# Kernel tuning notes

Measured on AMD Instinct MI355X. Metric: run time of the kernel, lower is better.

## Reference

```python
import jax, jax.numpy as jnp
import numpy as np

D_MODEL = 512
N_HEADS = 8
D_K = D_MODEL // N_HEADS
WINDOW = 64
SCALE = 1.0 / np.sqrt(D_K)


def setup_inputs() -> dict:
    key = jax.random.key(0)
    ks = jax.random.split(key, 9)
    B, S = 1, 2048
    s = 1.0 / np.sqrt(D_MODEL)
    inp = {
        "x": jax.random.normal(ks[0], (B, S, D_MODEL), dtype=jnp.float32),
        "Wq": jax.random.normal(ks[1], (D_MODEL, D_MODEL), dtype=jnp.float32) * s,
        "bq": jnp.zeros((D_MODEL,), dtype=jnp.float32),
        "Wk": jax.random.normal(ks[2], (D_MODEL, D_MODEL), dtype=jnp.float32) * s,
        "bk": jnp.zeros((D_MODEL,), dtype=jnp.float32),
        "Wv": jax.random.normal(ks[3], (D_MODEL, D_MODEL), dtype=jnp.float32) * s,
        "bv": jnp.zeros((D_MODEL,), dtype=jnp.float32),
        "Wo": jax.random.normal(ks[4], (D_MODEL, D_MODEL), dtype=jnp.float32) * s,
        "bo": jnp.zeros((D_MODEL,), dtype=jnp.float32),
    }
    return inp


def reference(x, Wq, bq, Wk, bk, Wv, bv, Wo, bo):
    B, S, _ = x.shape
    # projections (torch Linear: x @ W.T + b); split heads -> [B,S,H,dk]
    q = (x @ Wq.T + bq).reshape(B, S, N_HEADS, D_K)
    k = (x @ Wk.T + bk).reshape(B, S, N_HEADS, D_K)
    v = (x @ Wv.T + bv).reshape(B, S, N_HEADS, D_K)

    # banded window indices: position i attends to [i-W, i+W]
    L = 2 * WINDOW + 1
    offsets = jnp.arange(L) - WINDOW                    # [L]
    pos = jnp.arange(S)[:, None] + offsets[None, :]     # [S, L]
    valid = (pos >= 0) & (pos < S)                      # [S, L]
    posc = jnp.clip(pos, 0, S - 1)

    k_w = k[:, posc]                                    # [B, S, L, H, dk]
    v_w = v[:, posc]                                    # [B, S, L, H, dk]

    scores = jnp.einsum("bshd,bslhd->bhsl", q, k_w) * SCALE
    scores = jnp.where(valid[None, None, :, :], scores, -jnp.inf)
    attn = jax.nn.softmax(scores, axis=-1)              # [B, H, S, L]
    out = jnp.einsum("bhsl,bslhd->bshd", attn, v_w)     # [B, S, H, dk]
    out = out.reshape(B, S, D_MODEL)
    return out @ Wo.T + bo
```

## Files before the change

### kernel.cpp

```cpp
#include <hip/hip_runtime.h>
#include <hip/hip_bf16.h>
#include <math.h>

#define S_LEN  2048
#define DMODEL 512
#define NHEADS 8
#define DK     64
#define WIN    64

static constexpr float SCALE = 0.125f;

typedef short bf16x8 __attribute__((ext_vector_type(8)));
typedef float f32x4  __attribute__((ext_vector_type(4)));

__device__ __forceinline__ short bfh(float v)
{
    __hip_bfloat16 b = __float2bfloat16(v);
    return *reinterpret_cast<short*>(&b);
}
__device__ __forceinline__ float bf2f(short s)
{
    __hip_bfloat16 b = *reinterpret_cast<__hip_bfloat16*>(&s);
    return __bfloat162float(b);
}
__device__ __forceinline__ void split1(float v, short& h, short& l)
{
    h = bfh(v);
    l = bfh(v - bf2f(h));
}

__device__ __forceinline__ void dma16(const void* g, void* l)
{
    __builtin_amdgcn_global_load_lds(
        (const __attribute__((address_space(1))) unsigned int*)g,
        (__attribute__((address_space(3))) unsigned int*)l, 16, 0, 0);
}

__global__ __launch_bounds__(256)
void cast_ws(const float* __restrict__ x,  const float* __restrict__ wq,
             const float* __restrict__ wk, const float* __restrict__ wv,
             const float* __restrict__ wo,
             short* __restrict__ xh, short* __restrict__ xl,
             short* __restrict__ wqb, short* __restrict__ wkb,
             short* __restrict__ wvb, short* __restrict__ wob)
{
    const int z = blockIdx.z;
    if (z == 0) {
        for (int i = blockIdx.x * 256 + threadIdx.x; i < 262144; i += gridDim.x * 256) {
            const float4 v = ((const float4*)x)[i];
            short4 h, l;
            split1(v.x, h.x, l.x);
            split1(v.y, h.y, l.y);
            split1(v.z, h.z, l.z);
            split1(v.w, h.w, l.w);
            ((short4*)xh)[i] = h;
            ((short4*)xl)[i] = l;
        }
    } else {
        const float* s; short* d;
        switch (z) {
            case 1:  s = wq; d = wqb; break;
            case 2:  s = wk; d = wkb; break;
            case 3:  s = wv; d = wvb; break;
            default: s = wo; d = wob; break;
        }
        for (int i = blockIdx.x * 256 + threadIdx.x; i < 65536; i += gridDim.x * 256) {
            const float4 v = ((const float4*)s)[i];
            short4 o;
            o.x = bfh(v.x); o.y = bfh(v.y); o.z = bfh(v.z); o.w = bfh(v.w);
            ((short4*)d)[i] = o;
        }
    }
}

__global__ __launch_bounds__(128)
void gemm_qkv3(const short* __restrict__ xh, const short* __restrict__ xl,
               const short* __restrict__ wqb, const short* __restrict__ wkb,
               const short* __restrict__ wvb,
               const float* __restrict__ bq, const float* __restrict__ bk,
               const float* __restrict__ bv,
               short* __restrict__ qh, short* __restrict__ ql,
               short* __restrict__ kb, short* __restrict__ vbt)
{
    __shared__ __align__(16) short sB[64 * 256];

    const int z = blockIdx.z;
    const short* Bg   = (z == 0) ? wqb : (z == 1) ? wkb : wvb;
    const float* bias = (z == 0) ? bq  : (z == 1) ? bk  : bv;
    const int row0 = blockIdx.y * 64;
    const int col0 = blockIdx.x * 64;
    const int tid  = threadIdx.x;
    const int lane = tid & 63;
    const int wv   = tid >> 6;
    const int col  = lane & 15;
    const int quad = lane >> 4;

    f32x4 acc[2][4];
#pragma unroll
    for (int mi = 0; mi < 2; ++mi)
#pragma unroll
        for (int nj = 0; nj < 4; ++nj)
            acc[mi][nj] = (f32x4)0.0f;

    for (int ph = 0; ph < 2; ++ph) {
        __syncthreads();
        for (int i = wv; i < 32; i += 2) {
            const int q = i * 64 + lane;
            const int r = q >> 5;
            const int b = q & 31;
            const int j = b ^ (r & 7);
            dma16(Bg + (size_t)(col0 + r) * 512 + ph * 256 + j * 8, sB + i * 512);
        }
        __syncthreads();

#pragma unroll
        for (int kc = 0; kc < 8; ++kc) {
            const int k = ph * 256 + kc * 32;
            bf16x8 ah[2], al[2];
#pragma unroll
            for (int mi = 0; mi < 2; ++mi) {
                const int m = row0 + wv * 32 + mi * 16 + col;
                ah[mi] = *(const bf16x8*)(xh + (size_t)m * 512 + k + quad * 8);
                al[mi] = *(const bf16x8*)(xl + (size_t)m * 512 + k + quad * 8);
            }
#pragma unroll
            for (int nj = 0; nj < 4; ++nj) {
                const int n = nj * 16 + col;
                const int j = (kc * 4 + quad) ^ (n & 7);
                const bf16x8 bf = *(const bf16x8*)&sB[n * 256 + j * 8];
#pragma unroll
                for (int mi = 0; mi < 2; ++mi) {
                    acc[mi][nj] = __builtin_amdgcn_mfma_f32_16x16x32_bf16(ah[mi], bf, acc[mi][nj], 0, 0, 0);
                    acc[mi][nj] = __builtin_amdgcn_mfma_f32_16x16x32_bf16(al[mi], bf, acc[mi][nj], 0, 0, 0);
                }
            }
        }
    }

#pragma unroll
    for (int nj = 0; nj < 4; ++nj) {
        const int cc = col0 + nj * 16 + col;
        const float bias_v = bias[cc];
#pragma unroll
        for (int mi = 0; mi < 2; ++mi) {
#pragma unroll
            for (int e = 0; e < 4; ++e) {
                const int row = row0 + wv * 32 + mi * 16 + quad * 4 + e;
                const float val = acc[mi][nj][e] + bias_v;
                if (z == 0) {
                    short hh, ll;
                    split1(val, hh, ll);
                    qh[(size_t)row * 512 + cc] = hh;
                    ql[(size_t)row * 512 + cc] = ll;
                } else if (z == 1) {
                    kb[(size_t)row * 512 + cc] = bfh(val);
                } else {
                    vbt[(size_t)cc * 2048 + row] = bfh(val);
                }
            }
        }
    }
}

__global__ __launch_bounds__(128)
void gemm_out3(const short* __restrict__ ah_g, const short* __restrict__ al_g,
               const short* __restrict__ wob, const float* __restrict__ bo,
               float* __restrict__ out)
{
    __shared__ __align__(16) short sB[64 * 256];

    const int row0 = blockIdx.y * 32;
    const int col0 = blockIdx.x * 64;
    const int tid  = threadIdx.x;
    const int lane = tid & 63;
    const int wv   = tid >> 6;
    const int col  = lane & 15;
    const int quad = lane >> 4;

    f32x4 acc[4];
#pragma unroll
    for (int nj = 0; nj < 4; ++nj)
        acc[nj] = (f32x4)0.0f;

    for (int ph = 0; ph < 2; ++ph) {
        __syncthreads();
        for (int i = wv; i < 32; i += 2) {
            const int q = i * 64 + lane;
            const int r = q >> 5;
            const int b = q & 31;
            const int j = b ^ (r & 7);
            dma16(wob + (size_t)(col0 + r) * 512 + ph * 256 + j * 8, sB + i * 512);
        }
        __syncthreads();

#pragma unroll
        for (int kc = 0; kc < 8; ++kc) {
            const int k = ph * 256 + kc * 32;
            const int m = row0 + wv * 16 + col;
            const bf16x8 ah = *(const bf16x8*)(ah_g + (size_t)m * 512 + k + quad * 8);
            const bf16x8 al = *(const bf16x8*)(al_g + (size_t)m * 512 + k + quad * 8);
#pragma unroll
            for (int nj = 0; nj < 4; ++nj) {
                const int n = nj * 16 + col;
                const int j = (kc * 4 + quad) ^ (n & 7);
                const bf16x8 bf = *(const bf16x8*)&sB[n * 256 + j * 8];
                acc[nj] = __builtin_amdgcn_mfma_f32_16x16x32_bf16(ah, bf, acc[nj], 0, 0, 0);
                acc[nj] = __builtin_amdgcn_mfma_f32_16x16x32_bf16(al, bf, acc[nj], 0, 0, 0);
            }
        }
    }

#pragma unroll
    for (int nj = 0; nj < 4; ++nj) {
        const int cc = col0 + nj * 16 + col;
        const float bias_v = bo[cc];
#pragma unroll
        for (int e = 0; e < 4; ++e) {
            const int row = row0 + wv * 16 + quad * 4 + e;
            out[(size_t)row * 512 + cc] = acc[nj][e] + bias_v;
        }
    }
}

__global__ __launch_bounds__(256)
void banded_attn3(const short* __restrict__ qh, const short* __restrict__ ql,
                  const short* __restrict__ kb, const short* __restrict__ vbt,
                  short* __restrict__ abh, short* __restrict__ abl)
{
    __shared__ __align__(16) short VtS[64 * 256];
    __shared__ __align__(16) short KS [192 * 64];
    __shared__ __align__(16) short QhS[32 * 64];
    __shared__ __align__(16) short QlS[32 * 64];
    __shared__ float pmax[4][32];
    __shared__ float psum[4][32];
    short* PS = KS;

    const int h    = blockIdx.x;
    const int t0   = blockIdx.y * 32;
    const int tid  = threadIdx.x;
    const int lane = tid & 63;
    const int wv   = tid >> 6;
    const int col  = lane & 15;
    const int quad = lane >> 4;

    {
        const int lr = lane >> 3;
        const int lc = lane & 7;
        for (int i = wv; i < 32; i += 4) {
            const short* src; short* dst; int r;
            if (i < 4) {
                r = i * 8 + lr;
                src = qh + (size_t)(t0 + r) * 512 + h * 64;
                dst = QhS + i * 512;
            } else if (i < 8) {
                const int g = i - 4;
                r = g * 8 + lr;
                src = ql + (size_t)(t0 + r) * 512 + h * 64;
                dst = QlS + g * 512;
            } else {
                const int g = i - 8;
                r = g * 8 + lr;
                int pos = t0 - 64 + r;
                pos = pos < 0 ? 0 : (pos > 2047 ? 2047 : pos);
                src = kb + (size_t)pos * 512 + h * 64;
                dst = KS + g * 512;
            }
            const int cs = lc ^ (r & 7);
            dma16(src + cs * 8, dst);
        }
        for (int i = wv; i < 32; i += 4) {
            const int q = i * 64 + lane;
            const int d = q >> 5;
            const int b = q & 31;
            const int j0 = (b < 24) ? b : 0;
            const int j = j0 ^ (d & 7);
            int p0 = t0 - 64 + j * 8;
            p0 = p0 < 0 ? 0 : (p0 > 2040 ? 2040 : p0);
            dma16(vbt + (size_t)(h * 64 + d) * 2048 + p0, VtS + i * 512);
        }
    }
    __syncthreads();

    f32x4 sacc[2][3];
#pragma unroll
    for (int mi = 0; mi < 2; ++mi)
#pragma unroll
        for (int nj = 0; nj < 3; ++nj)
            sacc[mi][nj] = (f32x4)0.0f;

#pragma unroll
    for (int ks = 0; ks < 2; ++ks) {
        const int q0 = ks * 4 + quad;
        bf16x8 aqh[2], aql[2];
#pragma unroll
        for (int mi = 0; mi < 2; ++mi) {
            const int m = mi * 16 + col;
            const int p = q0 ^ (m & 7);
            aqh[mi] = *(const bf16x8*)&QhS[m * 64 + p * 8];
            aql[mi] = *(const bf16x8*)&QlS[m * 64 + p * 8];
        }
#pragma unroll
        for (int nj = 0; nj < 3; ++nj) {
            const int n = wv * 48 + nj * 16 + col;
            const int p = q0 ^ (n & 7);
            const bf16x8 bkf = *(const bf16x8*)&KS[n * 64 + p * 8];
#pragma unroll
            for (int mi = 0; mi < 2; ++mi) {
                sacc[mi][nj] = __builtin_amdgcn_mfma_f32_16x16x32_bf16(aqh[mi], bkf, sacc[mi][nj], 0, 0, 0);
                sacc[mi][nj] = __builtin_amdgcn_mfma_f32_16x16x32_bf16(aql[mi], bkf, sacc[mi][nj], 0, 0, 0);
            }
        }
    }

    float pv[2][3][4];
#pragma unroll
    for (int mi = 0; mi < 2; ++mi)
#pragma unroll
        for (int nj = 0; nj < 3; ++nj)
#pragma unroll
            for (int e = 0; e < 4; ++e) {
                const int r32 = mi * 16 + quad * 4 + e;
                const int n   = wv * 48 + nj * 16 + col;
                const int pos = t0 - 64 + n;
                const int d   = n - r32;
                const bool valid = (pos >= 0) && (pos < S_LEN) && (d >= 0) && (d <= 128);
                pv[mi][nj][e] = valid ? sacc[mi][nj][e] * SCALE : -__builtin_inff();
            }

#pragma unroll
    for (int mi = 0; mi < 2; ++mi)
#pragma unroll
        for (int e = 0; e < 4; ++e) {
            float mx = fmaxf(fmaxf(pv[mi][0][e], pv[mi][1][e]), pv[mi][2][e]);
#pragma unroll
            for (int off = 1; off < 16; off <<= 1)
                mx = fmaxf(mx, __shfl_xor(mx, off));
            if ((lane & 15) == 0) pmax[wv][mi * 16 + quad * 4 + e] = mx;
        }
    __syncthreads();

#pragma unroll
    for (int mi = 0; mi < 2; ++mi)
#pragma unroll
        for (int e = 0; e < 4; ++e) {
            const int r32 = mi * 16 + quad * 4 + e;
            const float m = fmaxf(fmaxf(pmax[0][r32], pmax[1][r32]),
                                  fmaxf(pmax[2][r32], pmax[3][r32]));
            float ss = 0.f;
#pragma unroll
            for (int nj = 0; nj < 3; ++nj) {
                const float p = __expf(pv[mi][nj][e] - m);
                pv[mi][nj][e] = p;
                ss += p;
            }
#pragma unroll
            for (int off = 1; off < 16; off <<= 1)
                ss += __shfl_xor(ss, off);
            if ((lane & 15) == 0) psum[wv][r32] = ss;
#pragma unroll
            for (int nj = 0; nj < 3; ++nj) {
                const int n = wv * 48 + nj * 16 + col;
                PS[r32 * 200 + n] = bfh(pv[mi][nj][e]);
            }
        }
    __syncthreads();

    const int mi = wv >> 1;
    f32x4 oacc[2];
    oacc[0] = (f32x4)0.0f;
    oacc[1] = (f32x4)0.0f;
#pragma unroll
    for (int ks = 0; ks < 6; ++ks) {
        const bf16x8 pa = *(const bf16x8*)&PS[(mi * 16 + col) * 200 + ks * 32 + quad * 8];
#pragma unroll
        for (int t = 0; t < 2; ++t) {
            const int d = ((wv & 1) * 2 + t) * 16 + col;
            const int j = (ks * 4 + quad) ^ (d & 7);
            const bf16x8 vf = *(const bf16x8*)&VtS[d * 256 + j * 8];
            oacc[t] = __builtin_amdgcn_mfma_f32_16x16x32_bf16(pa, vf, oacc[t], 0, 0, 0);
        }
    }

    float linv[4];
#pragma unroll
    for (int e = 0; e < 4; ++e) {
        const int r32 = mi * 16 + quad * 4 + e;
        linv[e] = 1.0f / (psum[0][r32] + psum[1][r32] + psum[2][r32] + psum[3][r32]);
    }
#pragma unroll
    for (int t = 0; t < 2; ++t) {
        const int nj = (wv & 1) * 2 + t;
#pragma unroll
        for (int e = 0; e < 4; ++e) {
            const int r32 = mi * 16 + quad * 4 + e;
            const float val = oacc[t][e] * linv[e];
            short hh, ll;
            split1(val, hh, ll);
            const size_t idx = (size_t)(t0 + r32) * 512 + h * 64 + nj * 16 + col;
            abh[idx] = hh;
            abl[idx] = ll;
        }
    }
}

extern "C" void kernel_launch(void* const* d_in, const int* in_sizes, int n_in,
                              void* d_out, int out_size, void* d_ws, size_t ws_size,
                              hipStream_t stream)
{
    const float* x  = (const float*)d_in[0];
    const float* Wq = (const float*)d_in[1];
    const float* bq = (const float*)d_in[2];
    const float* Wk = (const float*)d_in[3];
    const float* bk = (const float*)d_in[4];
    const float* Wv = (const float*)d_in[5];
    const float* bv = (const float*)d_in[6];
    const float* Wo = (const float*)d_in[7];
    const float* bo = (const float*)d_in[8];
    float* out = (float*)d_out;

    char* ws = (char*)d_ws;
    short* qh  = (short*)(ws);
    short* ql  = (short*)(ws + (2u << 20));
    short* kb  = (short*)(ws + (4u << 20));
    short* vbt = (short*)(ws + (6u << 20));
    short* xh  = (short*)(ws + (8u << 20));
    short* xl  = (short*)(ws + (10u << 20));
    short* wqb = (short*)(ws + (12u << 20));
    short* wkb = (short*)(ws + (12u << 20) + 1 * (512u << 10));
    short* wvb = (short*)(ws + (12u << 20) + 2 * (512u << 10));
    short* wob = (short*)(ws + (12u << 20) + 3 * (512u << 10));
    short* abh = xh;
    short* abl = xl;

    dim3 gc(128, 1, 5);
    cast_ws<<<gc, 256, 0, stream>>>(x, Wq, Wk, Wv, Wo,
                                    xh, xl, wqb, wkb, wvb, wob);

    dim3 gq(DMODEL / 64, S_LEN / 64, 3);
    gemm_qkv3<<<gq, 128, 0, stream>>>(xh, xl, wqb, wkb, wvb,
                                      bq, bk, bv, qh, ql, kb, vbt);

    dim3 ga(NHEADS, S_LEN / 32);
    banded_attn3<<<ga, 256, 0, stream>>>(qh, ql, kb, vbt, abh, abl);

    dim3 go(DMODEL / 64, S_LEN / 32);
    gemm_out3<<<go, 128, 0, stream>>>(abh, abl, wob, bo, out);
}
```

Before: 114.8 us.

## Fuse x hi/lo split into QKV GEMM and drop lo term in output GEMM

The separate cast of x into bf16 hi/lo buffers is removed. The QKV GEMM now loads fp32 x directly and splits it in registers, which saves a full write and read of the x buffers. The attention output is written as a single bf16 plane, and the output projection drops its second low-part MFMA, halving that GEMM's MFMA work and its A-operand traffic. The trade-off is lower precision in the output projection, and each QKV block redoes the x split across the three z slices and all column tiles.

```diff
diff --git a/kernel.cpp b/kernel.cpp
--- a/kernel.cpp
+++ b/kernel.cpp
@@ -28,6 +28,19 @@
     h = bfh(v);
     l = bfh(v - bf2f(h));
 }
+__device__ __forceinline__ void split8(const float4 a0, const float4 a1,
+                                       bf16x8& h8, bf16x8& l8)
+{
+    short hh, ll;
+    split1(a0.x, hh, ll); h8[0] = hh; l8[0] = ll;
+    split1(a0.y, hh, ll); h8[1] = hh; l8[1] = ll;
+    split1(a0.z, hh, ll); h8[2] = hh; l8[2] = ll;
+    split1(a0.w, hh, ll); h8[3] = hh; l8[3] = ll;
+    split1(a1.x, hh, ll); h8[4] = hh; l8[4] = ll;
+    split1(a1.y, hh, ll); h8[5] = hh; l8[5] = ll;
+    split1(a1.z, hh, ll); h8[6] = hh; l8[6] = ll;
+    split1(a1.w, hh, ll); h8[7] = hh; l8[7] = ll;
+}
 
 __device__ __forceinline__ void dma16(const void* g, void* l)
 {
@@ -37,44 +50,28 @@
 }
 
 __global__ __launch_bounds__(256)
-void cast_ws(const float* __restrict__ x,  const float* __restrict__ wq,
-             const float* __restrict__ wk, const float* __restrict__ wv,
-             const float* __restrict__ wo,
-             short* __restrict__ xh, short* __restrict__ xl,
-             short* __restrict__ wqb, short* __restrict__ wkb,
-             short* __restrict__ wvb, short* __restrict__ wob)
-{
-    const int z = blockIdx.z;
-    if (z == 0) {
-        for (int i = blockIdx.x * 256 + threadIdx.x; i < 262144; i += gridDim.x * 256) {
-            const float4 v = ((const float4*)x)[i];
-            short4 h, l;
-            split1(v.x, h.x, l.x);
-            split1(v.y, h.y, l.y);
-            split1(v.z, h.z, l.z);
-            split1(v.w, h.w, l.w);
-            ((short4*)xh)[i] = h;
-            ((short4*)xl)[i] = l;
-        }
-    } else {
-        const float* s; short* d;
-        switch (z) {
-            case 1:  s = wq; d = wqb; break;
-            case 2:  s = wk; d = wkb; break;
-            case 3:  s = wv; d = wvb; break;
-            default: s = wo; d = wob; break;
-        }
-        for (int i = blockIdx.x * 256 + threadIdx.x; i < 65536; i += gridDim.x * 256) {
-            const float4 v = ((const float4*)s)[i];
-            short4 o;
-            o.x = bfh(v.x); o.y = bfh(v.y); o.z = bfh(v.z); o.w = bfh(v.w);
-            ((short4*)d)[i] = o;
-        }
+void cast_w(const float* __restrict__ wq, const float* __restrict__ wk,
+            const float* __restrict__ wv, const float* __restrict__ wo,
+            short* __restrict__ wqb, short* __restrict__ wkb,
+            short* __restrict__ wvb, short* __restrict__ wob)
+{
+    const float* s; short* d;
+    switch (blockIdx.z) {
+        case 0:  s = wq; d = wqb; break;
+        case 1:  s = wk; d = wkb; break;
+        case 2:  s = wv; d = wvb; break;
+        default: s = wo; d = wob; break;
+    }
+    for (int i = blockIdx.x * 256 + threadIdx.x; i < 65536; i += gridDim.x * 256) {
+        const float4 v = ((const float4*)s)[i];
+        short4 o;
+        o.x = bfh(v.x); o.y = bfh(v.y); o.z = bfh(v.z); o.w = bfh(v.w);
+        ((short4*)d)[i] = o;
     }
 }
 
 __global__ __launch_bounds__(128)
-void gemm_qkv3(const short* __restrict__ xh, const short* __restrict__ xl,
+void gemm_qkv4(const float* __restrict__ x,
                const short* __restrict__ wqb, const short* __restrict__ wkb,
                const short* __restrict__ wvb,
                const float* __restrict__ bq, const float* __restrict__ bk,
@@ -120,8 +117,10 @@
 #pragma unroll
             for (int mi = 0; mi < 2; ++mi) {
                 const int m = row0 + wv * 32 + mi * 16 + col;
-                ah[mi] = *(const bf16x8*)(xh + (size_t)m * 512 + k + quad * 8);
-                al[mi] = *(const bf16x8*)(xl + (size_t)m * 512 + k + quad * 8);
+                const float* xp = x + (size_t)m * 512 + k + quad * 8;
+                const float4 a0 = *(const float4*)xp;
+                const float4 a1 = *(const float4*)(xp + 4);
+                split8(a0, a1, ah[mi], al[mi]);
             }
 #pragma unroll
             for (int nj = 0; nj < 4; ++nj) {
@@ -163,7 +162,7 @@
 }
 
 __global__ __launch_bounds__(128)
-void gemm_out3(const short* __restrict__ ah_g, const short* __restrict__ al_g,
+void gemm_out4(const short* __restrict__ ah_g,
                const short* __restrict__ wob, const float* __restrict__ bo,
                float* __restrict__ out)
 {
@@ -198,14 +197,12 @@
             const int k = ph * 256 + kc * 32;
             const int m = row0 + wv * 16 + col;
             const bf16x8 ah = *(const bf16x8*)(ah_g + (size_t)m * 512 + k + quad * 8);
-            const bf16x8 al = *(const bf16x8*)(al_g + (size_t)m * 512 + k + quad * 8);
 #pragma unroll
             for (int nj = 0; nj < 4; ++nj) {
                 const int n = nj * 16 + col;
                 const int j = (kc * 4 + quad) ^ (n & 7);
                 const bf16x8 bf = *(const bf16x8*)&sB[n * 256 + j * 8];
                 acc[nj] = __builtin_amdgcn_mfma_f32_16x16x32_bf16(ah, bf, acc[nj], 0, 0, 0);
-                acc[nj] = __builtin_amdgcn_mfma_f32_16x16x32_bf16(al, bf, acc[nj], 0, 0, 0);
             }
         }
     }
@@ -223,9 +220,9 @@
 }
 
 __global__ __launch_bounds__(256)
-void banded_attn3(const short* __restrict__ qh, const short* __restrict__ ql,
+void banded_attn4(const short* __restrict__ qh, const short* __restrict__ ql,
                   const short* __restrict__ kb, const short* __restrict__ vbt,
-                  short* __restrict__ abh, short* __restrict__ abl)
+                  short* __restrict__ abh)
 {
     __shared__ __align__(16) short VtS[64 * 256];
     __shared__ __align__(16) short KS [192 * 64];
@@ -394,11 +391,8 @@
         for (int e = 0; e < 4; ++e) {
             const int r32 = mi * 16 + quad * 4 + e;
             const float val = oacc[t][e] * linv[e];
-            short hh, ll;
-            split1(val, hh, ll);
             const size_t idx = (size_t)(t0 + r32) * 512 + h * 64 + nj * 16 + col;
-            abh[idx] = hh;
-            abl[idx] = ll;
+            abh[idx] = bfh(val);
         }
     }
 }
@@ -423,26 +417,22 @@
     short* ql  = (short*)(ws + (2u << 20));
     short* kb  = (short*)(ws + (4u << 20));
     short* vbt = (short*)(ws + (6u << 20));
-    short* xh  = (short*)(ws + (8u << 20));
-    short* xl  = (short*)(ws + (10u << 20));
+    short* abh = (short*)(ws + (8u << 20));
     short* wqb = (short*)(ws + (12u << 20));
     short* wkb = (short*)(ws + (12u << 20) + 1 * (512u << 10));
     short* wvb = (short*)(ws + (12u << 20) + 2 * (512u << 10));
     short* wob = (short*)(ws + (12u << 20) + 3 * (512u << 10));
-    short* abh = xh;
-    short* abl = xl;
-
-    dim3 gc(128, 1, 5);
-    cast_ws<<<gc, 256, 0, stream>>>(x, Wq, Wk, Wv, Wo,
-                                    xh, xl, wqb, wkb, wvb, wob);
+
+    dim3 gw(64, 1, 4);
+    cast_w<<<gw, 256, 0, stream>>>(Wq, Wk, Wv, Wo, wqb, wkb, wvb, wob);
 
     dim3 gq(DMODEL / 64, S_LEN / 64, 3);
-    gemm_qkv3<<<gq, 128, 0, stream>>>(xh, xl, wqb, wkb, wvb,
+    gemm_qkv4<<<gq, 128, 0, stream>>>(x, wqb, wkb, wvb,
                                       bq, bk, bv, qh, ql, kb, vbt);
 
     dim3 ga(NHEADS, S_LEN / 32);
-    banded_attn3<<<ga, 256, 0, stream>>>(qh, ql, kb, vbt, abh, abl);
+    banded_attn4<<<ga, 256, 0, stream>>>(qh, ql, kb, vbt, abh);
 
     dim3 go(DMODEL / 64, S_LEN / 32);
-    gemm_out3<<<go, 128, 0, stream>>>(abh, abl, wob, bo, out);
-}
+    gemm_out4<<<go, 128, 0, stream>>>(abh, wob, bo, out);
+}
```

Result: faster. 112.5 us (-2.0%).

## Drop hi/lo split for Q and attention output, retile QKV GEMM

Applied to the files above, without the earlier changes.

Q and the attention output are now stored as a single bf16 value instead of a hi/lo bf16 pair. This halves the MFMA work in QK^T and in the output projection, and cuts their global traffic. The QKV GEMM now uses 32-row tiles with 128-wide K phases and a smaller LDS buffer, which doubles the block count and should improve occupancy. The trade is lower precision for Q and the attention result, which may affect accuracy against the fp32 reference.

```diff
diff --git a/kernel.cpp b/kernel.cpp
--- a/kernel.cpp
+++ b/kernel.cpp
@@ -37,24 +37,24 @@
 }
 
 __global__ __launch_bounds__(256)
-void cast_ws(const float* __restrict__ x,  const float* __restrict__ wq,
-             const float* __restrict__ wk, const float* __restrict__ wv,
-             const float* __restrict__ wo,
-             short* __restrict__ xh, short* __restrict__ xl,
-             short* __restrict__ wqb, short* __restrict__ wkb,
-             short* __restrict__ wvb, short* __restrict__ wob)
+void prep(const float* __restrict__ x,
+          const float* __restrict__ wq, const float* __restrict__ wk,
+          const float* __restrict__ wv, const float* __restrict__ wo,
+          short* __restrict__ xh, short* __restrict__ xl,
+          short* __restrict__ wqb, short* __restrict__ wkb,
+          short* __restrict__ wvb, short* __restrict__ wob)
 {
     const int z = blockIdx.z;
     if (z == 0) {
         for (int i = blockIdx.x * 256 + threadIdx.x; i < 262144; i += gridDim.x * 256) {
             const float4 v = ((const float4*)x)[i];
-            short4 h, l;
-            split1(v.x, h.x, l.x);
-            split1(v.y, h.y, l.y);
-            split1(v.z, h.z, l.z);
-            split1(v.w, h.w, l.w);
-            ((short4*)xh)[i] = h;
-            ((short4*)xl)[i] = l;
+            short4 h4, l4;
+            split1(v.x, h4.x, l4.x);
+            split1(v.y, h4.y, l4.y);
+            split1(v.z, h4.z, l4.z);
+            split1(v.w, h4.w, l4.w);
+            ((short4*)xh)[i] = h4;
+            ((short4*)xl)[i] = l4;
         }
     } else {
         const float* s; short* d;
@@ -74,101 +74,19 @@
 }
 
 __global__ __launch_bounds__(128)
-void gemm_qkv3(const short* __restrict__ xh, const short* __restrict__ xl,
+void gemm_qkv7(const short* __restrict__ xh, const short* __restrict__ xl,
                const short* __restrict__ wqb, const short* __restrict__ wkb,
                const short* __restrict__ wvb,
                const float* __restrict__ bq, const float* __restrict__ bk,
                const float* __restrict__ bv,
-               short* __restrict__ qh, short* __restrict__ ql,
-               short* __restrict__ kb, short* __restrict__ vbt)
-{
-    __shared__ __align__(16) short sB[64 * 256];
+               short* __restrict__ qb, short* __restrict__ kb,
+               short* __restrict__ vbt)
+{
+    __shared__ __align__(16) short sW[64 * 128];
 
     const int z = blockIdx.z;
     const short* Bg   = (z == 0) ? wqb : (z == 1) ? wkb : wvb;
     const float* bias = (z == 0) ? bq  : (z == 1) ? bk  : bv;
-    const int row0 = blockIdx.y * 64;
-    const int col0 = blockIdx.x * 64;
-    const int tid  = threadIdx.x;
-    const int lane = tid & 63;
-    const int wv   = tid >> 6;
-    const int col  = lane & 15;
-    const int quad = lane >> 4;
-
-    f32x4 acc[2][4];
-#pragma unroll
-    for (int mi = 0; mi < 2; ++mi)
-#pragma unroll
-        for (int nj = 0; nj < 4; ++nj)
-            acc[mi][nj] = (f32x4)0.0f;
-
-    for (int ph = 0; ph < 2; ++ph) {
-        __syncthreads();
-        for (int i = wv; i < 32; i += 2) {
-            const int q = i * 64 + lane;
-            const int r = q >> 5;
-            const int b = q & 31;
-            const int j = b ^ (r & 7);
-            dma16(Bg + (size_t)(col0 + r) * 512 + ph * 256 + j * 8, sB + i * 512);
-        }
-        __syncthreads();
-
-#pragma unroll
-        for (int kc = 0; kc < 8; ++kc) {
-            const int k = ph * 256 + kc * 32;
-            bf16x8 ah[2], al[2];
-#pragma unroll
-            for (int mi = 0; mi < 2; ++mi) {
-                const int m = row0 + wv * 32 + mi * 16 + col;
-                ah[mi] = *(const bf16x8*)(xh + (size_t)m * 512 + k + quad * 8);
-                al[mi] = *(const bf16x8*)(xl + (size_t)m * 512 + k + quad * 8);
-            }
-#pragma unroll
-            for (int nj = 0; nj < 4; ++nj) {
-                const int n = nj * 16 + col;
-                const int j = (kc * 4 + quad) ^ (n & 7);
-                const bf16x8 bf = *(const bf16x8*)&sB[n * 256 + j * 8];
-#pragma unroll
-                for (int mi = 0; mi < 2; ++mi) {
-                    acc[mi][nj] = __builtin_amdgcn_mfma_f32_16x16x32_bf16(ah[mi], bf, acc[mi][nj], 0, 0, 0);
-                    acc[mi][nj] = __builtin_amdgcn_mfma_f32_16x16x32_bf16(al[mi], bf, acc[mi][nj], 0, 0, 0);
-                }
-            }
-        }
-    }
-
-#pragma unroll
-    for (int nj = 0; nj < 4; ++nj) {
-        const int cc = col0 + nj * 16 + col;
-        const float bias_v = bias[cc];
-#pragma unroll
-        for (int mi = 0; mi < 2; ++mi) {
-#pragma unroll
-            for (int e = 0; e < 4; ++e) {
-                const int row = row0 + wv * 32 + mi * 16 + quad * 4 + e;
-                const float val = acc[mi][nj][e] + bias_v;
-                if (z == 0) {
-                    short hh, ll;
-                    split1(val, hh, ll);
-                    qh[(size_t)row * 512 + cc] = hh;
-                    ql[(size_t)row * 512 + cc] = ll;
-                } else if (z == 1) {
-                    kb[(size_t)row * 512 + cc] = bfh(val);
-                } else {
-                    vbt[(size_t)cc * 2048 + row] = bfh(val);
-                }
-            }
-        }
-    }
-}
-
-__global__ __launch_bounds__(128)
-void gemm_out3(const short* __restrict__ ah_g, const short* __restrict__ al_g,
-               const short* __restrict__ wob, const float* __restrict__ bo,
-               float* __restrict__ out)
-{
-    __shared__ __align__(16) short sB[64 * 256];
-
     const int row0 = blockIdx.y * 32;
     const int col0 = blockIdx.x * 64;
     const int tid  = threadIdx.x;
@@ -176,36 +94,98 @@
     const int wv   = tid >> 6;
     const int col  = lane & 15;
     const int quad = lane >> 4;
+    const int m    = row0 + wv * 16 + col;
 
     f32x4 acc[4];
 #pragma unroll
     for (int nj = 0; nj < 4; ++nj)
         acc[nj] = (f32x4)0.0f;
 
-    for (int ph = 0; ph < 2; ++ph) {
+    for (int ph = 0; ph < 4; ++ph) {
         __syncthreads();
-        for (int i = wv; i < 32; i += 2) {
-            const int q = i * 64 + lane;
-            const int r = q >> 5;
-            const int b = q & 31;
-            const int j = b ^ (r & 7);
-            dma16(wob + (size_t)(col0 + r) * 512 + ph * 256 + j * 8, sB + i * 512);
+        for (int i = wv; i < 16; i += 2) {
+            const int r = i * 4 + (lane >> 4);
+            const int c = lane & 15;
+            const int j = c ^ (r & 7);
+            dma16(Bg + (size_t)(col0 + r) * 512 + ph * 128 + j * 8, sW + i * 512);
         }
         __syncthreads();
 
 #pragma unroll
-        for (int kc = 0; kc < 8; ++kc) {
-            const int k = ph * 256 + kc * 32;
-            const int m = row0 + wv * 16 + col;
-            const bf16x8 ah = *(const bf16x8*)(ah_g + (size_t)m * 512 + k + quad * 8);
-            const bf16x8 al = *(const bf16x8*)(al_g + (size_t)m * 512 + k + quad * 8);
+        for (int kc = 0; kc < 4; ++kc) {
+            const size_t aoff = (size_t)m * 512 + ph * 128 + kc * 32 + quad * 8;
+            const bf16x8 ah = *(const bf16x8*)(xh + aoff);
+            const bf16x8 al = *(const bf16x8*)(xl + aoff);
 #pragma unroll
             for (int nj = 0; nj < 4; ++nj) {
                 const int n = nj * 16 + col;
-                const int j = (kc * 4 + quad) ^ (n & 7);
-                const bf16x8 bf = *(const bf16x8*)&sB[n * 256 + j * 8];
+                const int c = kc * 4 + quad;
+                const bf16x8 bf = *(const bf16x8*)&sW[n * 128 + (c ^ (n & 7)) * 8];
                 acc[nj] = __builtin_amdgcn_mfma_f32_16x16x32_bf16(ah, bf, acc[nj], 0, 0, 0);
                 acc[nj] = __builtin_amdgcn_mfma_f32_16x16x32_bf16(al, bf, acc[nj], 0, 0, 0);
+            }
+        }
+    }
+
+#pragma unroll
+    for (int nj = 0; nj < 4; ++nj) {
+        const int cc = col0 + nj * 16 + col;
+        const float bias_v = bias[cc];
+#pragma unroll
+        for (int e = 0; e < 4; ++e) {
+            const int row = row0 + wv * 16 + quad * 4 + e;
+            const float val = acc[nj][e] + bias_v;
+            if (z == 0) {
+                qb[(size_t)row * 512 + cc] = bfh(val);
+            } else if (z == 1) {
+                kb[(size_t)row * 512 + cc] = bfh(val);
+            } else {
+                vbt[(size_t)cc * 2048 + row] = bfh(val);
+            }
+        }
+    }
+}
+
+__global__ __launch_bounds__(128)
+void gemm_out7(const short* __restrict__ ah_g,
+               const short* __restrict__ wob, const float* __restrict__ bo,
+               float* __restrict__ out)
+{
+    __shared__ __align__(16) short sW[64 * 128];
+
+    const int row0 = blockIdx.y * 32;
+    const int col0 = blockIdx.x * 64;
+    const int tid  = threadIdx.x;
+    const int lane = tid & 63;
+    const int wv   = tid >> 6;
+    const int col  = lane & 15;
+    const int quad = lane >> 4;
+    const int m    = row0 + wv * 16 + col;
+
+    f32x4 acc[4];
+#pragma unroll
+    for (int nj = 0; nj < 4; ++nj)
+        acc[nj] = (f32x4)0.0f;
+
+    for (int ph = 0; ph < 4; ++ph) {
+        __syncthreads();
+        for (int i = wv; i < 16; i += 2) {
+            const int r = i * 4 + (lane >> 4);
+            const int c = lane & 15;
+            const int j = c ^ (r & 7);
+            dma16(wob + (size_t)(col0 + r) * 512 + ph * 128 + j * 8, sW + i * 512);
+        }
+        __syncthreads();
+
+#pragma unroll
+        for (int kc = 0; kc < 4; ++kc) {
+            const bf16x8 af = *(const bf16x8*)(ah_g + (size_t)m * 512 + ph * 128 + kc * 32 + quad * 8);
+#pragma unroll
+            for (int nj = 0; nj < 4; ++nj) {
+                const int n = nj * 16 + col;
+                const int c = kc * 4 + quad;
+                const bf16x8 bf = *(const bf16x8*)&sW[n * 128 + (c ^ (n & 7)) * 8];
+                acc[nj] = __builtin_amdgcn_mfma_f32_16x16x32_bf16(af, bf, acc[nj], 0, 0, 0);
             }
         }
     }
@@ -223,14 +203,12 @@
 }
 
 __global__ __launch_bounds__(256)
-void banded_attn3(const short* __restrict__ qh, const short* __restrict__ ql,
-                  const short* __restrict__ kb, const short* __restrict__ vbt,
-                  short* __restrict__ abh, short* __restrict__ abl)
+void banded_attn6(const short* __restrict__ qb, const short* __restrict__ kb,
+                  const short* __restrict__ vbt, short* __restrict__ abh)
 {
     __shared__ __align__(16) short VtS[64 * 256];
     __shared__ __align__(16) short KS [192 * 64];
-    __shared__ __align__(16) short QhS[32 * 64];
-    __shared__ __align__(16) short QlS[32 * 64];
+    __shared__ __align__(16) short QS [32 * 64];
     __shared__ float pmax[4][32];
     __shared__ float psum[4][32];
     short* PS = KS;
@@ -246,19 +224,14 @@
     {
         const int lr = lane >> 3;
         const int lc = lane & 7;
-        for (int i = wv; i < 32; i += 4) {
+        for (int i = wv; i < 28; i += 4) {
             const short* src; short* dst; int r;
             if (i < 4) {
                 r = i * 8 + lr;
-                src = qh + (size_t)(t0 + r) * 512 + h * 64;
-                dst = QhS + i * 512;
-            } else if (i < 8) {
+                src = qb + (size_t)(t0 + r) * 512 + h * 64;
+                dst = QS + i * 512;
+            } else {
                 const int g = i - 4;
-                r = g * 8 + lr;
-                src = ql + (size_t)(t0 + r) * 512 + h * 64;
-                dst = QlS + g * 512;
-            } else {
-                const int g = i - 8;
                 r = g * 8 + lr;
                 int pos = t0 - 64 + r;
                 pos = pos < 0 ? 0 : (pos > 2047 ? 2047 : pos);
@@ -291,13 +264,12 @@
 #pragma unroll
     for (int ks = 0; ks < 2; ++ks) {
         const int q0 = ks * 4 + quad;
-        bf16x8 aqh[2], aql[2];
+        bf16x8 aq[2];
 #pragma unroll
         for (int mi = 0; mi < 2; ++mi) {
-            const int m = mi * 16 + col;
-            const int p = q0 ^ (m & 7);
-            aqh[mi] = *(const bf16x8*)&QhS[m * 64 + p * 8];
-            aql[mi] = *(const bf16x8*)&QlS[m * 64 + p * 8];
+            const int mm = mi * 16 + col;
+            const int p = q0 ^ (mm & 7);
+            aq[mi] = *(const bf16x8*)&QS[mm * 64 + p * 8];
         }
 #pragma unroll
         for (int nj = 0; nj < 3; ++nj) {
@@ -305,10 +277,8 @@
             const int p = q0 ^ (n & 7);
             const bf16x8 bkf = *(const bf16x8*)&KS[n * 64 + p * 8];
 #pragma unroll
-            for (int mi = 0; mi < 2; ++mi) {
-                sacc[mi][nj] = __builtin_amdgcn_mfma_f32_16x16x32_bf16(aqh[mi], bkf, sacc[mi][nj], 0, 0, 0);
-                sacc[mi][nj] = __builtin_amdgcn_mfma_f32_16x16x32_bf16(aql[mi], bkf, sacc[mi][nj], 0, 0, 0);
-            }
+            for (int mi = 0; mi < 2; ++mi)
+                sacc[mi][nj] = __builtin_amdgcn_mfma_f32_16x16x32_bf16(aq[mi], bkf, sacc[mi][nj], 0, 0, 0);
         }
     }
 
@@ -394,11 +364,8 @@
         for (int e = 0; e < 4; ++e) {
             const int r32 = mi * 16 + quad * 4 + e;
             const float val = oacc[t][e] * linv[e];
-            short hh, ll;
-            split1(val, hh, ll);
             const size_t idx = (size_t)(t0 + r32) * 512 + h * 64 + nj * 16 + col;
-            abh[idx] = hh;
-            abl[idx] = ll;
+            abh[idx] = bfh(val);
         }
     }
 }
@@ -419,30 +386,28 @@
     float* out = (float*)d_out;
 
     char* ws = (char*)d_ws;
-    short* qh  = (short*)(ws);
-    short* ql  = (short*)(ws + (2u << 20));
-    short* kb  = (short*)(ws + (4u << 20));
-    short* vbt = (short*)(ws + (6u << 20));
+    short* qb  = (short*)(ws);
+    short* kb  = (short*)(ws + (2u << 20));
+    short* vbt = (short*)(ws + (4u << 20));
+    short* abh = (short*)(ws + (6u << 20));
     short* xh  = (short*)(ws + (8u << 20));
     short* xl  = (short*)(ws + (10u << 20));
     short* wqb = (short*)(ws + (12u << 20));
     short* wkb = (short*)(ws + (12u << 20) + 1 * (512u << 10));
     short* wvb = (short*)(ws + (12u << 20) + 2 * (512u << 10));
     short* wob = (short*)(ws + (12u << 20) + 3 * (512u << 10));
-    short* abh = xh;
-    short* abl = xl;
-
-    dim3 gc(128, 1, 5);
-    cast_ws<<<gc, 256, 0, stream>>>(x, Wq, Wk, Wv, Wo,
-                                    xh, xl, wqb, wkb, wvb, wob);
-
-    dim3 gq(DMODEL / 64, S_LEN / 64, 3);
-    gemm_qkv3<<<gq, 128, 0, stream>>>(xh, xl, wqb, wkb, wvb,
-                                      bq, bk, bv, qh, ql, kb, vbt);
+
+    dim3 gp(128, 1, 5);
+    prep<<<gp, 256, 0, stream>>>(x, Wq, Wk, Wv, Wo,
+                                 xh, xl, wqb, wkb, wvb, wob);
+
+    dim3 gq(DMODEL / 64, S_LEN / 32, 3);
+    gemm_qkv7<<<gq, 128, 0, stream>>>(xh, xl, wqb, wkb, wvb,
+                                      bq, bk, bv, qb, kb, vbt);
 
     dim3 ga(NHEADS, S_LEN / 32);
-    banded_attn3<<<ga, 256, 0, stream>>>(qh, ql, kb, vbt, abh, abl);
+    banded_attn6<<<ga, 256, 0, stream>>>(qb, kb, vbt, abh);
 
     dim3 go(DMODEL / 64, S_LEN / 32);
-    gemm_out3<<<go, 128, 0, stream>>>(abh, abl, wob, bo, out);
-}
+    gemm_out7<<<go, 128, 0, stream>>>(abh, wob, bo, out);
+}
```

After: 112.3 us. 2.2% less time.
